# Kernel optimization log

Hardware: AMD Instinct MI355X
Metric: run time of the kernel (lower is better)

The kernel has to match this reference:

```python
import jax, jax.numpy as jnp
import numpy as np

N, T, HW = 32, 46, 128
VOCAB_Q, NUM_ANS = 96, 32
WVEC, RNN_DIM = 32, 128
CNN_DIM, G_DIM, F_DIM = 24, 256, 256
G_IN = 2 * (CNN_DIM + 2) + RNN_DIM  # 180
BN_EPS = 1e-5


def setup_inputs() -> dict:
    key = jax.random.key(0)
    ks = jax.random.split(key, 16)
    s = 0.05
    rn = lambda k, shape: jax.random.normal(k, shape, dtype=jnp.float32) * s
    z = lambda shape: jnp.zeros(shape, jnp.float32)
    o = lambda shape: jnp.ones(shape, jnp.float32)
    inp = {}
    inp['questions'] = jax.random.randint(ks[0], (N, T), 1, VOCAB_Q)  # no NULL padding -> last step is the valid hidden state
    inp['images'] = jax.random.normal(ks[1], (N, 3, HW, HW), dtype=jnp.float32)
    inp['embed_W'] = rn(ks[2], (VOCAB_Q, WVEC))
    inp['lstm_Wih'] = rn(ks[3], (4 * RNN_DIM, WVEC))
    inp['lstm_Whh'] = rn(ks[4], (4 * RNN_DIM, RNN_DIM))
    inp['lstm_bih'] = z((4 * RNN_DIM,))
    inp['lstm_bhh'] = z((4 * RNN_DIM,))
    inp['conv0_W'] = rn(ks[5], (CNN_DIM, 3, 3, 3))
    inp['conv0_b'] = z((CNN_DIM,))
    inp['bn0_g'] = o((CNN_DIM,))
    inp['bn0_b'] = z((CNN_DIM,))
    inp['convs_W'] = rn(ks[6], (3, CNN_DIM, CNN_DIM, 3, 3))
    inp['convs_b'] = z((3, CNN_DIM))
    inp['bns_g'] = o((3, CNN_DIM))
    inp['bns_b'] = z((3, CNN_DIM))
    inp['g0_W'] = rn(ks[7], (G_DIM, G_IN))
    inp['g0_b'] = z((G_DIM,))
    inp['gs_W'] = rn(ks[8], (3, G_DIM, G_DIM))
    inp['gs_b'] = z((3, G_DIM))
    inp['f0_W'] = rn(ks[9], (F_DIM, G_DIM))
    inp['f0_b'] = z((F_DIM,))
    inp['f1_W'] = rn(ks[10], (F_DIM, F_DIM))
    inp['f1_b'] = z((F_DIM,))
    inp['f2_W'] = rn(ks[11], (NUM_ANS, F_DIM))
    inp['f2_b'] = z((NUM_ANS,))
    return inp


def _dense(x, W, b):
    return x @ W.T + b


def _lstm_last(emb, Wih, Whh, bih, bhh):
    # emb: (N, T, D); single-layer LSTM, PyTorch gate order (i, f, g, o); return last hidden state
    n, h = emb.shape[0], Whh.shape[1]
    bias = bih + bhh

    def step(carry, x_t):
        hp, cp = carry
        zg = x_t @ Wih.T + hp @ Whh.T + bias
        i, f, g, o_ = jnp.split(zg, 4, axis=-1)
        c = jax.nn.sigmoid(f) * cp + jax.nn.sigmoid(i) * jnp.tanh(g)
        hn = jax.nn.sigmoid(o_) * jnp.tanh(c)
        return (hn, c), None

    init = (jnp.zeros((n, h), emb.dtype), jnp.zeros((n, h), emb.dtype))
    (h_last, _), _ = jax.lax.scan(step, init, jnp.swapaxes(emb, 0, 1))
    return h_last


def _conv_bn_relu(x, W, b, gamma, beta):
    # Conv2d(k=3, s=2, p=1) + BatchNorm2d (training-mode batch stats) + ReLU
    x = jax.lax.conv_general_dilated(x, W, window_strides=(2, 2), padding=((1, 1), (1, 1)),
                                     dimension_numbers=('NCHW', 'OIHW', 'NCHW'))
    x = x + b[None, :, None, None]
    mu = x.mean((0, 2, 3), keepdims=True)
    var = ((x - mu) ** 2).mean((0, 2, 3), keepdims=True)  # biased var, as torch BN
    x = (x - mu) * jax.lax.rsqrt(var + BN_EPS)
    x = x * gamma[None, :, None, None] + beta[None, :, None, None]
    return jax.nn.relu(x)


def _forward(questions, images, embed_W, lstm_Wih, lstm_Whh, lstm_bih, lstm_bhh,
             conv0_W, conv0_b, bn0_g, bn0_b, convs_W, convs_b, bns_g, bns_b,
             g0_W, g0_b, gs_W, gs_b, f0_W, f0_b, f1_W, f1_b, f2_W, f2_b):
    # question encoder
    q_feats = _lstm_last(embed_W[questions], lstm_Wih, lstm_Whh, lstm_bih, lstm_bhh)  # (N, rnn_dim)
    # CNN stem
    x = _conv_bn_relu(images, conv0_W, conv0_b, bn0_g, bn0_b)
    for i in range(3):
        x = _conv_bn_relu(x, convs_W[i], convs_b[i], bns_g[i], bns_b[i])
    n, c, h, w = x.shape
    m = h * w
    # append normalized coordinates
    xc = jnp.broadcast_to(jnp.linspace(0.0, 1.0, w, dtype=x.dtype).reshape(1, 1, 1, w), (n, 1, h, w))
    yc = jnp.broadcast_to(jnp.linspace(0.0, 1.0, h, dtype=x.dtype).reshape(1, 1, h, 1), (n, 1, h, w))
    objects = jnp.concatenate([x, xc, yc], axis=1).reshape(n, c + 2, m)
    objects = jnp.swapaxes(objects, 1, 2)  # (N, M, C+2)
    # all M^2 ordered pairs: pairs[n, i*M+j] = [obj_i, obj_j]
    feats1 = jnp.repeat(objects, m, axis=1)        # (N, M^2, C+2)
    feats2 = jnp.tile(objects, (1, m, 1))          # (N, M^2, C+2)
    q_rep = jnp.broadcast_to(q_feats[:, None, :], (n, m * m, q_feats.shape[-1]))
    g_in = jnp.concatenate([feats1, feats2, q_rep], axis=-1)  # (N, M^2, 180)
    # shared MLP g
    hidden = jax.nn.relu(_dense(g_in, g0_W, g0_b))
    for i in range(3):
        hidden = jax.nn.relu(_dense(hidden, gs_W[i], gs_b[i]))
    f_in = hidden.sum(axis=1)  # old-torch sum(1) kept dim then [:,0] -> (N, g_dim)
    # MLP f (dropout = identity at eval)
    hidden = jax.nn.relu(_dense(f_in, f0_W, f0_b))
    hidden = jax.nn.relu(_dense(hidden, f1_W, f1_b))
    return _dense(hidden, f2_W, f2_b)  # (N, num_answers)


def reference(questions, images, embed_W, lstm_Wih, lstm_Whh, lstm_bih, lstm_bhh,
              conv0_W, conv0_b, bn0_g, bn0_b, convs_W, convs_b, bns_g, bns_b,
              g0_W, g0_b, gs_W, gs_b, f0_W, f0_b, f1_W, f1_b, f2_W, f2_b):
    return _forward(questions, images, embed_W, lstm_Wih, lstm_Whh, lstm_bih, lstm_bhh,
                    conv0_W, conv0_b, bn0_g, bn0_b, convs_W, convs_b, bns_g, bns_b,
                    g0_W, g0_b, gs_W, gs_b, f0_W, f0_b, f1_W, f1_b, f2_W, f2_b)
```

## Files before the change

kernel.cpp:

```cpp
#include <hip/hip_runtime.h>

#define NB   32
#define TT   46
#define RNN  128
#define CDIM 24
#define GD   256
#define GIN  180

typedef __attribute__((ext_vector_type(8))) short  bf16x8;
typedef __attribute__((ext_vector_type(4))) short  s16x4;
typedef __attribute__((ext_vector_type(8))) unsigned short u16x8;
typedef __attribute__((ext_vector_type(4))) float  f32x4;

__device__ __forceinline__ unsigned short f2bf(float v) {
    unsigned u = __float_as_uint(v);
    u = u + 0x7fffu + ((u >> 16) & 1u);
    return (unsigned short)(u >> 16);
}

__device__ __forceinline__ void lstm_body(
    const int* __restrict__ q, const float* __restrict__ embW,
    const float* __restrict__ Wih, const float* __restrict__ Whh,
    const float* __restrict__ bih, const float* __restrict__ bhh,
    float* __restrict__ qf, int n)
{
    const int tid = threadIdx.x;
    __shared__ __align__(16) float xs[32], hs[RNN];
    __shared__ float zg[512];
    f32x4 wih[8], whh[32];
    {
        const f32x4* wp = (const f32x4*)(Wih + tid * 32);
#pragma unroll
        for (int j = 0; j < 8; j++) wih[j] = wp[j];
        const f32x4* hp = (const f32x4*)(Whh + tid * RNN);
#pragma unroll
        for (int j = 0; j < 32; j++) whh[j] = hp[j];
    }
    const float bias = bih[tid] + bhh[tid];
    float creg = 0.f;
    if (tid < RNN) hs[tid] = 0.f;
    float xr = (tid < 32) ? embW[q[n * TT] * 32 + tid] : 0.f;
    __syncthreads();
    for (int t = 0; t < TT; t++) {
        if (tid < 32) xs[tid] = xr;
        __syncthreads();
        if (tid < 32 && t + 1 < TT) xr = embW[q[n * TT + t + 1] * 32 + tid];
        const f32x4* h4 = (const f32x4*)hs;
        const f32x4* x4 = (const f32x4*)xs;
        f32x4 a0 = {0.f, 0.f, 0.f, 0.f}, a1 = a0, a2 = a0, a3 = a0;
#pragma unroll
        for (int j = 0; j < 8; j += 4) {
            a0 += wih[j] * x4[j];     a1 += wih[j + 1] * x4[j + 1];
            a2 += wih[j + 2] * x4[j + 2]; a3 += wih[j + 3] * x4[j + 3];
        }
#pragma unroll
        for (int j = 0; j < 32; j += 4) {
            a0 += whh[j] * h4[j];     a1 += whh[j + 1] * h4[j + 1];
            a2 += whh[j + 2] * h4[j + 2]; a3 += whh[j + 3] * h4[j + 3];
        }
        f32x4 a = (a0 + a1) + (a2 + a3);
        zg[tid] = bias + ((a[0] + a[1]) + (a[2] + a[3]));
        __syncthreads();
        if (tid < RNN) {
            float ig = 1.f / (1.f + __expf(-zg[tid]));
            float fg = 1.f / (1.f + __expf(-zg[RNN + tid]));
            float gg = tanhf(zg[2 * RNN + tid]);
            float og = 1.f / (1.f + __expf(-zg[3 * RNN + tid]));
            float cn = fg * creg + ig * gg;
            creg = cn;
            hs[tid] = og * tanhf(cn);
        }
        __syncthreads();
    }
    if (tid < RNN) qf[n * RNN + tid] = hs[tid];
}

template<int CIN, int TILE, bool BNIN, int BS>
__device__ __forceinline__ void conv_body(
    const float* __restrict__ in, const float* __restrict__ Wg,
    const float* __restrict__ bias,
    const float* __restrict__ pstats, const float* __restrict__ pg,
    const float* __restrict__ pb, float pinvM,
    float* __restrict__ out, float* __restrict__ stats,
    int HIN, int WIN, int HO, int WO, int tilesX, int bx)
{
    constexpr int NPIX = TILE * TILE;
    constexpr int CPG  = BS / NPIX;
    constexpr int COPT = 24 / CPG;
    constexpr int WPB  = BS / 64;
    constexpr int WPC  = NPIX / 64;
    constexpr int S  = 2 * TILE + 1;
    constexpr int SP = S + 1;
    __shared__ float in_t[CIN][S][SP];
    __shared__ float r1s[WPB][COPT], r2s[WPB][COPT];
    __shared__ float sc[CIN], sh[CIN];
    const int tid = threadIdx.x;
    const int tx = bx % tilesX;
    const int ty = (bx / tilesX) % tilesX;
    const int n  = bx / (tilesX * tilesX);

    if (BNIN) {
        if (tid < CIN) {
            float mu  = pstats[2 * tid] * pinvM;
            float var = pstats[2 * tid + 1] * pinvM - mu * mu;
            float rs  = rsqrtf(var + 1e-5f);
            sc[tid] = rs * pg[tid];
            sh[tid] = pb[tid] - mu * rs * pg[tid];
        }
        __syncthreads();
    }
    const int iy0 = ty * 2 * TILE - 1, ix0 = tx * 2 * TILE - 1;
    for (int idx = tid; idx < CIN * S * S; idx += BS) {
        int ci = idx / (S * S), r = idx % (S * S);
        int ry = r / S, rx = r % S;
        int gy = iy0 + ry, gx = ix0 + rx;
        float v = 0.f;
        if ((unsigned)gy < (unsigned)HIN && (unsigned)gx < (unsigned)WIN) {
            v = in[((size_t)(n * CIN + ci) * HIN + gy) * WIN + gx];
            if (BNIN) v = fmaxf(v * sc[ci] + sh[ci], 0.f);
        }
        in_t[ci][ry][rx] = v;
    }
    __syncthreads();

    const int p   = tid % NPIX;
    const int co0 = __builtin_amdgcn_readfirstlane((tid / NPIX) * COPT);
    const int ly  = (p / TILE) * 2, lx = (p % TILE) * 2;
    float acc[COPT];
#pragma unroll
    for (int c = 0; c < COPT; c++) acc[c] = bias[co0 + c];
    for (int ci = 0; ci < CIN; ci++) {
#pragma unroll
        for (int ky = 0; ky < 3; ky++) {
            const float* row = &in_t[ci][ly + ky][lx];
#pragma unroll
            for (int kx = 0; kx < 3; kx++) {
                float v = row[kx];
#pragma unroll
                for (int c = 0; c < COPT; c++)
                    acc[c] += v * Wg[(((co0 + c) * CIN + ci) * 3 + ky) * 3 + kx];
            }
        }
    }
    const int oy = ty * TILE + p / TILE, ox = tx * TILE + p % TILE;
#pragma unroll
    for (int c = 0; c < COPT; c++)
        out[((size_t)(n * 24 + co0 + c) * HO + oy) * WO + ox] = acc[c];

    const int lane = tid & 63, wv = tid >> 6;
#pragma unroll
    for (int c = 0; c < COPT; c++) {
        float s1 = acc[c], s2 = acc[c] * acc[c];
#pragma unroll
        for (int off = 1; off < 64; off <<= 1) {
            s1 += __shfl_xor(s1, off, 64);
            s2 += __shfl_xor(s2, off, 64);
        }
        if (lane == 0) { r1s[wv][c] = s1; r2s[wv][c] = s2; }
    }
    __syncthreads();
    if (tid < 24) {
        int cg = tid / COPT, slot = tid % COPT;
        float t1 = 0.f, t2 = 0.f;
#pragma unroll
        for (int u = 0; u < WPC; u++) { t1 += r1s[cg * WPC + u][slot]; t2 += r2s[cg * WPC + u][slot]; }
        atomicAdd(&stats[tid * 2],     t1);
        atomicAdd(&stats[tid * 2 + 1], t2);
    }
}

template<int CIN, int TILE, bool BNIN>
__global__ __launch_bounds__(256) void conv_tiled(
    const float* __restrict__ in, const float* __restrict__ Wg,
    const float* __restrict__ bias,
    const float* __restrict__ pstats, const float* __restrict__ pg,
    const float* __restrict__ pb, float pinvM,
    float* __restrict__ out, float* __restrict__ stats,
    int HIN, int WIN, int HO, int WO, int tilesX)
{
    conv_body<CIN, TILE, BNIN, 256>(in, Wg, bias, pstats, pg, pb, pinvM,
                                    out, stats, HIN, WIN, HO, WO, tilesX, blockIdx.x);
}

__global__ __launch_bounds__(512, 2) void fused_front(
    const int* __restrict__ q, const float* __restrict__ embW,
    const float* __restrict__ Wih, const float* __restrict__ Whh,
    const float* __restrict__ bih, const float* __restrict__ bhh,
    float* __restrict__ qf,
    const float* __restrict__ images, const float* __restrict__ c0W,
    const float* __restrict__ c0b, float* __restrict__ conv0o,
    float* __restrict__ stats,
    const float* __restrict__ gsW, unsigned short* __restrict__ Wbf)
{
    const int bx = blockIdx.x;
    if (bx < 32) {
        lstm_body(q, embW, Wih, Whh, bih, bhh, qf, bx);
    } else if (bx < 544) {
        conv_body<3, 16, false, 512>(images, c0W, c0b, nullptr, nullptr, nullptr, 0.f,
                                     conv0o, stats, 128, 128, 64, 64, 4, bx - 32);
    } else {
        int i = ((bx - 544) << 9) + threadIdx.x;
#pragma unroll
        for (int u = 0; u < 4; u++) {
            Wbf[i] = f2bf(gsW[i]);
            i += 96 * 512;
        }
    }
}

__global__ __launch_bounds__(256) void abqt_kernel(
    const float* __restrict__ feat,
    const float* __restrict__ stats, const float* __restrict__ g,
    const float* __restrict__ b, float invM,
    const float* __restrict__ qf,
    const float* __restrict__ g0W,
    const float* __restrict__ g0b,
    float* __restrict__ A, float* __restrict__ Bm, float* __restrict__ QT)
{
    const int n = blockIdx.x >> 2, iq = blockIdx.x & 3, k = threadIdx.x;
    __shared__ float wAB[256][53];
    __shared__ float wq[64][128];
    __shared__ float obj[16][28];
    __shared__ float qs[RNN];
    __shared__ float sc[24], sh[24];
    if (k < 24) {
        float mu  = stats[2 * k] * invM;
        float var = stats[2 * k + 1] * invM - mu * mu;
        float rs  = rsqrtf(var + 1e-5f);
        sc[k] = rs * g[k];
        sh[k] = b[k] - mu * rs * g[k];
    }
    if (k >= 128) qs[k - 128] = qf[n * RNN + (k - 128)];
    for (int idx = k; idx < 256 * 52; idx += 256) {
        int kr = idx / 52, c = idx % 52;
        wAB[kr][c] = g0W[kr * GIN + c];
    }
    for (int idx = k; idx < 64 * 128; idx += 256) {
        int r = idx >> 7, d = idx & 127;
        wq[r][d] = g0W[(((iq << 6) + r)) * GIN + 52 + d];
    }
    __syncthreads();
    for (int idx = k; idx < 24 * 16; idx += 256) {
        int c = idx >> 4, il = idx & 15;
        int i = (iq << 4) + il;
        float v = feat[(n * CDIM + c) * 64 + i];
        obj[il][c] = fmaxf(v * sc[c] + sh[c], 0.f);
    }
    if (k < 16) {
        int i = (iq << 4) + k;
        obj[k][24] = (float)(i & 7)  * (1.f / 7.f);
        obj[k][25] = (float)(i >> 3) * (1.f / 7.f);
        obj[k][26] = 0.f; obj[k][27] = 0.f;
    }
    __syncthreads();
    if (k < 64) {
        int kr = (iq << 6) + k;
        float qv = g0b[kr];
#pragma unroll
        for (int d = 0; d < RNN; d++) qv += wq[k][d] * qs[d];
        QT[(n << 8) + kr] = qv;
    }
    float wA[26], wB[26];
#pragma unroll
    for (int c = 0; c < 26; c++) { wA[c] = wAB[k][c]; wB[c] = wAB[k][26 + c]; }
    for (int il = 0; il < 16; il++) {
        const f32x4* op = (const f32x4*)obj[il];
        f32x4 r0 = op[0], r1 = op[1], r2 = op[2], r3 = op[3],
              r4 = op[4], r5 = op[5], r6 = op[6];
        float a = 0.f, bb = 0.f;
#pragma unroll
        for (int p = 0; p < 4; p++) {
            a += wA[p] * r0[p] + wA[4 + p] * r1[p] + wA[8 + p] * r2[p]
               + wA[12 + p] * r3[p] + wA[16 + p] * r4[p] + wA[20 + p] * r5[p];
            bb += wB[p] * r0[p] + wB[4 + p] * r1[p] + wB[8 + p] * r2[p]
                + wB[12 + p] * r3[p] + wB[16 + p] * r4[p] + wB[20 + p] * r5[p];
        }
        a += wA[24] * r6[0] + wA[25] * r6[1];
        bb += wB[24] * r6[0] + wB[25] * r6[1];
        int i = (iq << 4) + il;
        A [(((n << 6) + i) << 8) + k] = a;
        Bm[(((n << 6) + i) << 8) + k] = bb;
    }
}

__global__ __launch_bounds__(256, 2) void gs_fused(
    const float* __restrict__ A, const float* __restrict__ Bm, const float* __restrict__ QT,
    const unsigned short* __restrict__ Wb,
    const float* __restrict__ gsb,
    float* __restrict__ partial)
{
    __shared__ __align__(16) unsigned short Xs[128 * 256];
    __shared__ float AQ[2][256];
    __shared__ float biasv[3][256];
    const int raw = blockIdx.x;
    const int bb = (raw & 7) * 128 + (raw >> 3);
    const int n = bb >> 5, ip = bb & 31, tid = threadIdx.x;
    const int lane = tid & 63, w = tid >> 6, l15 = lane & 15, lh = lane >> 4;

    {
        float qt = QT[(n << 8) + tid];
        AQ[0][tid] = A[(((n << 6) + ip * 2)     << 8) + tid] + qt;
        AQ[1][tid] = A[(((n << 6) + ip * 2 + 1) << 8) + tid] + qt;
        biasv[0][tid] = gsb[tid];
        biasv[1][tid] = gsb[256 + tid];
        biasv[2][tid] = gsb[512 + tid];
    }
    __syncthreads();

#pragma unroll
    for (int it = 0; it < 16; it++) {
        int task = tid + (it << 8);
        int r = task >> 5, g = task & 31;
        int isub = r >> 6, j = r & 63;
        const f32x4* bp = (const f32x4*)(Bm + (((n << 6) + j) << 8) + (g << 3));
        f32x4 b0 = bp[0], b1 = bp[1];
        u16x8 pk;
        int c0 = g << 3;
#pragma unroll
        for (int p = 0; p < 4; p++) {
            pk[p]     = f2bf(fmaxf(b0[p] + AQ[isub][c0 + p], 0.f));
            pk[p + 4] = f2bf(fmaxf(b1[p] + AQ[isub][c0 + 4 + p], 0.f));
        }
        *(u16x8*)((char*)Xs + r * 512 + ((g ^ (r & 7)) << 4)) = pk;
    }

    f32x4 acc[4][8];
    const f32x4 zero4 = {0.f, 0.f, 0.f, 0.f};
    bf16x8 wa[4], wn[4], xa[8], xn[8];
    for (int layer = 0; layer < 3; layer++) {
#pragma unroll
        for (int tc = 0; tc < 4; tc++)
#pragma unroll
            for (int sl = 0; sl < 8; sl++) acc[tc][sl] = zero4;
        const unsigned short* wbase = Wb + (layer << 16)
                                    + (((w << 6) + l15) << 8) + (lh << 3);
#pragma unroll
        for (int tc = 0; tc < 4; tc++) wa[tc] = *(const bf16x8*)(wbase + (tc << 12));
        __syncthreads();
#pragma unroll
        for (int sl = 0; sl < 8; sl++) {
            int ar = (sl << 4) + l15;
            int au = lh ^ (ar & 7);
            xa[sl] = *(const bf16x8*)((const char*)Xs + ar * 512 + (au << 4));
        }
#pragma unroll
        for (int kb = 0; kb < 8; kb++) {
            if (kb < 7) {
#pragma unroll
                for (int tc = 0; tc < 4; tc++)
                    wn[tc] = *(const bf16x8*)(wbase + (tc << 12) + ((kb + 1) << 5));
#pragma unroll
                for (int sl = 0; sl < 8; sl++) {
                    int ar = (sl << 4) + l15;
                    int au = (((kb + 1) << 2) + lh) ^ (ar & 7);
                    xn[sl] = *(const bf16x8*)((const char*)Xs + ar * 512 + (au << 4));
                }
            }
#pragma unroll
            for (int tc = 0; tc < 4; tc++)
#pragma unroll
                for (int sl = 0; sl < 8; sl++)
                    acc[tc][sl] = __builtin_amdgcn_mfma_f32_16x16x32_bf16(
                        wa[tc], xa[sl], acc[tc][sl], 0, 0, 0);
            if (kb < 7) {
#pragma unroll
                for (int tc = 0; tc < 4; tc++) wa[tc] = wn[tc];
#pragma unroll
                for (int sl = 0; sl < 8; sl++) xa[sl] = xn[sl];
            }
        }
        if (layer < 2) {
            __syncthreads();
#pragma unroll
            for (int tc = 0; tc < 4; tc++) {
                int c0 = (w << 6) + (tc << 4) + (lh << 2);
                float b0 = biasv[layer][c0],     b1 = biasv[layer][c0 + 1];
                float b2 = biasv[layer][c0 + 2], b3 = biasv[layer][c0 + 3];
#pragma unroll
                for (int sl = 0; sl < 8; sl++) {
                    int row = (sl << 4) + l15;
                    s16x4 pk;
                    pk[0] = (short)f2bf(fmaxf(acc[tc][sl][0] + b0, 0.f));
                    pk[1] = (short)f2bf(fmaxf(acc[tc][sl][1] + b1, 0.f));
                    pk[2] = (short)f2bf(fmaxf(acc[tc][sl][2] + b2, 0.f));
                    pk[3] = (short)f2bf(fmaxf(acc[tc][sl][3] + b3, 0.f));
                    *(s16x4*)((char*)Xs + row * 512 + (((c0 >> 3) ^ (row & 7)) << 4)
                              + ((c0 & 7) << 1)) = pk;
                }
            }
        } else {
#pragma unroll
            for (int tc = 0; tc < 4; tc++) {
                int c0 = (w << 6) + (tc << 4) + (lh << 2);
                f32x4 cs;
#pragma unroll
                for (int p = 0; p < 4; p++) {
                    float bv = biasv[2][c0 + p];
                    float s = 0.f;
#pragma unroll
                    for (int sl = 0; sl < 8; sl++) s += fmaxf(acc[tc][sl][p] + bv, 0.f);
                    s += __shfl_xor(s, 1, 64);
                    s += __shfl_xor(s, 2, 64);
                    s += __shfl_xor(s, 4, 64);
                    s += __shfl_xor(s, 8, 64);
                    cs[p] = s;
                }
                if (l15 == 0) *(f32x4*)(partial + (size_t)bb * 256 + c0) = cs;
            }
        }
    }
}

__device__ __forceinline__ float dot256(const float* __restrict__ wr,
                                        const float* __restrict__ x)
{
    const f32x4* w4 = (const f32x4*)wr;
    const f32x4* x4 = (const f32x4*)x;
    f32x4 a0 = {0.f, 0.f, 0.f, 0.f}, a1 = a0, a2 = a0, a3 = a0;
#pragma unroll 8
    for (int c = 0; c < 64; c += 4) {
        f32x4 w0 = w4[c], w1 = w4[c + 1], w2 = w4[c + 2], w3 = w4[c + 3];
        f32x4 x0 = x4[c], x1 = x4[c + 1], x2 = x4[c + 2], x3 = x4[c + 3];
        a0 += w0 * x0; a1 += w1 * x1; a2 += w2 * x2; a3 += w3 * x3;
    }
    f32x4 a = (a0 + a1) + (a2 + a3);
    return (a[0] + a[1]) + (a[2] + a[3]);
}

__global__ __launch_bounds__(256) void f_mlp(
    const float* __restrict__ partial,
    const float* __restrict__ f0W, const float* __restrict__ f0b,
    const float* __restrict__ f1W, const float* __restrict__ f1b,
    const float* __restrict__ f2W, const float* __restrict__ f2b,
    float* __restrict__ out)
{
    const int n = blockIdx.x, k = threadIdx.x;
    __shared__ float fin[256], h1[256], h2[256];
    const float* pb = partial + (size_t)(n * 32) * 256 + k;
    float s0 = 0.f, s1 = 0.f, s2 = 0.f, s3 = 0.f;
#pragma unroll
    for (int b = 0; b < 32; b += 4) {
        s0 += pb[(b + 0) << 8];
        s1 += pb[(b + 1) << 8];
        s2 += pb[(b + 2) << 8];
        s3 += pb[(b + 3) << 8];
    }
    fin[k] = (s0 + s1) + (s2 + s3);
    __syncthreads();
    h1[k] = fmaxf(dot256(f0W + (k << 8), fin) + f0b[k], 0.f);
    __syncthreads();
    h2[k] = fmaxf(dot256(f1W + (k << 8), h1) + f1b[k], 0.f);
    __syncthreads();
    if (k < 32)
        out[(n << 5) + k] = dot256(f2W + (k << 8), h2) + f2b[k];
}

extern "C" void kernel_launch(void* const* d_in, const int* in_sizes, int n_in,
                              void* d_out, int out_size, void* d_ws, size_t ws_size,
                              hipStream_t stream)
{
    const int*   questions = (const int*)  d_in[0];
    const float* images = (const float*)d_in[1];
    const float* embW   = (const float*)d_in[2];
    const float* Wih    = (const float*)d_in[3];
    const float* Whh    = (const float*)d_in[4];
    const float* bih    = (const float*)d_in[5];
    const float* bhh    = (const float*)d_in[6];
    const float* c0W    = (const float*)d_in[7];
    const float* c0b    = (const float*)d_in[8];
    const float* bn0g   = (const float*)d_in[9];
    const float* bn0b   = (const float*)d_in[10];
    const float* csW    = (const float*)d_in[11];
    const float* csb    = (const float*)d_in[12];
    const float* bnsg   = (const float*)d_in[13];
    const float* bnsb   = (const float*)d_in[14];
    const float* g0W    = (const float*)d_in[15];
    const float* g0b    = (const float*)d_in[16];
    const float* gsW    = (const float*)d_in[17];
    const float* gsb    = (const float*)d_in[18];
    const float* f0W    = (const float*)d_in[19];
    const float* f0b    = (const float*)d_in[20];
    const float* f1W    = (const float*)d_in[21];
    const float* f1b    = (const float*)d_in[22];
    const float* f2W    = (const float*)d_in[23];
    const float* f2b    = (const float*)d_in[24];

    float* ws  = (float*)d_ws;
    float* out = (float*)d_out;

    float* conv0o = ws;
    float* conv1o = ws + 3145728;
    float* conv2o = ws + 3932160;
    float* conv3o = ws + 4128768;
    float* stats  = ws + 4177920;
    float* qf     = ws + 4178112;
    unsigned short* Wbf = (unsigned short*)(ws + 4182208);
    float* Abuf   = ws;
    float* Bbuf   = ws + 524288;
    float* QTb    = ws + 1048576;
    float* part   = ws + 1155072;

    hipMemsetAsync(stats, 0, 192 * sizeof(float), stream);

    fused_front<<<640, 512, 0, stream>>>(questions, embW, Wih, Whh, bih, bhh, qf,
                                         images, c0W, c0b, conv0o, stats, gsW, Wbf);
    conv_tiled<24, 8, true><<<512, 256, 0, stream>>>(
        conv0o, csW, csb, stats, bn0g, bn0b, 1.f / 131072.f,
        conv1o, stats + 48, 64, 64, 32, 32, 4);
    conv_tiled<24, 8, true><<<128, 256, 0, stream>>>(
        conv1o, csW + 5184, csb + 24, stats + 48, bnsg, bnsb, 1.f / 32768.f,
        conv2o, stats + 96, 32, 32, 16, 16, 2);
    conv_tiled<24, 8, true><<<32, 256, 0, stream>>>(
        conv2o, csW + 10368, csb + 48, stats + 96, bnsg + 24, bnsb + 24, 1.f / 8192.f,
        conv3o, stats + 144, 16, 16, 8, 8, 1);

    abqt_kernel<<<128, 256, 0, stream>>>(conv3o, stats + 144, bnsg + 48, bnsb + 48,
                                         1.f / 2048.f, qf, g0W, g0b, Abuf, Bbuf, QTb);
    gs_fused<<<1024, 256, 0, stream>>>(Abuf, Bbuf, QTb, Wbf, gsb, part);
    f_mlp<<<32, 256, 0, stream>>>(part, f0W, f0b, f1W, f1b, f2W, f2b, out);
}
```

Before: 276.7 us.

## Retile gs_fused MFMA work into 2x2 wave grid over rows and columns

Each wave now computes a 64-row by 128-column tile instead of all 128 rows by 64 columns. Per k-step a wave loads 8 weight fragments and 4 activation fragments from LDS, where before it loaded 4 and 8. The final row-sum is combined across the two row-half waves through a new shared buffer and an extra barrier. This shifts load pressure from LDS to global/L2 weight reads, keeps the accumulator count unchanged, and adds a small reduction step.

```diff
diff --git a/kernel.cpp b/kernel.cpp
--- a/kernel.cpp
+++ b/kernel.cpp
@@ -292,10 +292,12 @@
     __shared__ __align__(16) unsigned short Xs[128 * 256];
     __shared__ float AQ[2][256];
     __shared__ float biasv[3][256];
+    __shared__ float red[2][256];
     const int raw = blockIdx.x;
     const int bb = (raw & 7) * 128 + (raw >> 3);
     const int n = bb >> 5, ip = bb & 31, tid = threadIdx.x;
     const int lane = tid & 63, w = tid >> 6, l15 = lane & 15, lh = lane >> 4;
+    const int rh = w >> 1, ch = w & 1;
 
     {
         float qt = QT[(n << 8) + tid];
@@ -324,22 +326,22 @@
         *(u16x8*)((char*)Xs + r * 512 + ((g ^ (r & 7)) << 4)) = pk;
     }
 
-    f32x4 acc[4][8];
+    f32x4 acc[8][4];
     const f32x4 zero4 = {0.f, 0.f, 0.f, 0.f};
-    bf16x8 wa[4], wn[4], xa[8], xn[8];
+    bf16x8 wa[8], wn[8], xa[4], xn[4];
     for (int layer = 0; layer < 3; layer++) {
 #pragma unroll
-        for (int tc = 0; tc < 4; tc++)
-#pragma unroll
-            for (int sl = 0; sl < 8; sl++) acc[tc][sl] = zero4;
+        for (int tc = 0; tc < 8; tc++)
+#pragma unroll
+            for (int sl = 0; sl < 4; sl++) acc[tc][sl] = zero4;
         const unsigned short* wbase = Wb + (layer << 16)
-                                    + (((w << 6) + l15) << 8) + (lh << 3);
-#pragma unroll
-        for (int tc = 0; tc < 4; tc++) wa[tc] = *(const bf16x8*)(wbase + (tc << 12));
+                                    + (((ch << 7) + l15) << 8) + (lh << 3);
+#pragma unroll
+        for (int tc = 0; tc < 8; tc++) wa[tc] = *(const bf16x8*)(wbase + (tc << 12));
         __syncthreads();
 #pragma unroll
-        for (int sl = 0; sl < 8; sl++) {
-            int ar = (sl << 4) + l15;
+        for (int sl = 0; sl < 4; sl++) {
+            int ar = (rh << 6) + (sl << 4) + l15;
             int au = lh ^ (ar & 7);
             xa[sl] = *(const bf16x8*)((const char*)Xs + ar * 512 + (au << 4));
         }
@@ -347,66 +349,67 @@
         for (int kb = 0; kb < 8; kb++) {
             if (kb < 7) {
 #pragma unroll
-                for (int tc = 0; tc < 4; tc++)
+                for (int tc = 0; tc < 8; tc++)
                     wn[tc] = *(const bf16x8*)(wbase + (tc << 12) + ((kb + 1) << 5));
 #pragma unroll
-                for (int sl = 0; sl < 8; sl++) {
-                    int ar = (sl << 4) + l15;
+                for (int sl = 0; sl < 4; sl++) {
+                    int ar = (rh << 6) + (sl << 4) + l15;
                     int au = (((kb + 1) << 2) + lh) ^ (ar & 7);
                     xn[sl] = *(const bf16x8*)((const char*)Xs + ar * 512 + (au << 4));
                 }
             }
 #pragma unroll
-            for (int tc = 0; tc < 4; tc++)
-#pragma unroll
-                for (int sl = 0; sl < 8; sl++)
+            for (int tc = 0; tc < 8; tc++)
+#pragma unroll
+                for (int sl = 0; sl < 4; sl++)
                     acc[tc][sl] = __builtin_amdgcn_mfma_f32_16x16x32_bf16(
                         wa[tc], xa[sl], acc[tc][sl], 0, 0, 0);
             if (kb < 7) {
 #pragma unroll
-                for (int tc = 0; tc < 4; tc++) wa[tc] = wn[tc];
-#pragma unroll
-                for (int sl = 0; sl < 8; sl++) xa[sl] = xn[sl];
+                for (int tc = 0; tc < 8; tc++) wa[tc] = wn[tc];
+#pragma unroll
+                for (int sl = 0; sl < 4; sl++) xa[sl] = xn[sl];
             }
         }
         if (layer < 2) {
             __syncthreads();
 #pragma unroll
-            for (int tc = 0; tc < 4; tc++) {
-                int c0 = (w << 6) + (tc << 4) + (lh << 2);
-                float b0 = biasv[layer][c0],     b1 = biasv[layer][c0 + 1];
-                float b2 = biasv[layer][c0 + 2], b3 = biasv[layer][c0 + 3];
-#pragma unroll
-                for (int sl = 0; sl < 8; sl++) {
-                    int row = (sl << 4) + l15;
+            for (int tc = 0; tc < 8; tc++) {
+                int c0 = (ch << 7) + (tc << 4) + (lh << 2);
+                f32x4 bv = *(const f32x4*)&biasv[layer][c0];
+#pragma unroll
+                for (int sl = 0; sl < 4; sl++) {
+                    int row = (rh << 6) + (sl << 4) + l15;
                     s16x4 pk;
-                    pk[0] = (short)f2bf(fmaxf(acc[tc][sl][0] + b0, 0.f));
-                    pk[1] = (short)f2bf(fmaxf(acc[tc][sl][1] + b1, 0.f));
-                    pk[2] = (short)f2bf(fmaxf(acc[tc][sl][2] + b2, 0.f));
-                    pk[3] = (short)f2bf(fmaxf(acc[tc][sl][3] + b3, 0.f));
+                    pk[0] = (short)f2bf(fmaxf(acc[tc][sl][0] + bv[0], 0.f));
+                    pk[1] = (short)f2bf(fmaxf(acc[tc][sl][1] + bv[1], 0.f));
+                    pk[2] = (short)f2bf(fmaxf(acc[tc][sl][2] + bv[2], 0.f));
+                    pk[3] = (short)f2bf(fmaxf(acc[tc][sl][3] + bv[3], 0.f));
                     *(s16x4*)((char*)Xs + row * 512 + (((c0 >> 3) ^ (row & 7)) << 4)
                               + ((c0 & 7) << 1)) = pk;
                 }
             }
         } else {
 #pragma unroll
-            for (int tc = 0; tc < 4; tc++) {
-                int c0 = (w << 6) + (tc << 4) + (lh << 2);
+            for (int tc = 0; tc < 8; tc++) {
+                int c0 = (ch << 7) + (tc << 4) + (lh << 2);
+                f32x4 bv = *(const f32x4*)&biasv[2][c0];
                 f32x4 cs;
 #pragma unroll
                 for (int p = 0; p < 4; p++) {
-                    float bv = biasv[2][c0 + p];
                     float s = 0.f;
 #pragma unroll
-                    for (int sl = 0; sl < 8; sl++) s += fmaxf(acc[tc][sl][p] + bv, 0.f);
+                    for (int sl = 0; sl < 4; sl++) s += fmaxf(acc[tc][sl][p] + bv[p], 0.f);
                     s += __shfl_xor(s, 1, 64);
                     s += __shfl_xor(s, 2, 64);
                     s += __shfl_xor(s, 4, 64);
                     s += __shfl_xor(s, 8, 64);
                     cs[p] = s;
                 }
-                if (l15 == 0) *(f32x4*)(partial + (size_t)bb * 256 + c0) = cs;
+                if (l15 == 0) *(f32x4*)&red[rh][c0] = cs;
             }
+            __syncthreads();
+            partial[(size_t)bb * 256 + tid] = red[0][tid] + red[1][tid];
         }
     }
 }
```

Result: slower. 327.3 us (+18.3%).
